# Optimization experiments

Hardware: AMD Instinct MI355X
Metric: run time of the kernel (lower is better)

## Reference

```python
import jax, jax.numpy as jnp
import numpy as np

B, H, S = 64, 1024, 512
MIN_VAL, MAX_VAL = -1.0, 1.0
EPS = 1e-8  # torch F.cosine_similarity default eps


def setup_inputs() -> dict:
    key = jax.random.key(0)
    k1, k2, k3 = jax.random.split(key, 3)
    tree_state = jax.random.normal(k1, (B, H), dtype=jnp.float32)
    seq_states = jax.random.normal(k2, (B, H, S), dtype=jnp.float32)
    # binary validity mask (float, as it is multiplied in)
    seq_mask = (jax.random.uniform(k3, (B, S)) < 0.9).astype(jnp.float32)
    return {"tree_state": tree_state, "seq_states": seq_states, "seq_mask": seq_mask}


def reference(tree_state, seq_states, seq_mask):
    # scan over the seq axis; carry h: (B, H)
    xs = (jnp.transpose(seq_states, (2, 0, 1)), seq_mask.T)  # (S,B,H), (S,B)

    def step(h, x):
        s, m = x  # s: (B,H), m: (B,)
        dot = jnp.sum(h * s, axis=-1)  # (B,)
        denom = jnp.maximum(
            jnp.linalg.norm(h, axis=-1) * jnp.linalg.norm(s, axis=-1), EPS
        )
        cos = (dot / denom)[:, None]  # (B,1)
        h_new = jnp.clip(h + (s - h * cos) * m[:, None], MIN_VAL, MAX_VAL)
        return h_new, None

    h, _ = jax.lax.scan(step, tree_state, xs)
    return h
```

## Files before the change

kernel.cpp:

```cpp
#include <hip/hip_runtime.h>


#define NB 64
#define NH 1024
#define NS 512
#define EL 16

typedef float v4f __attribute__((ext_vector_type(4)));

template <int CTRL>
__device__ __forceinline__ float dpp_add(float x) {
  int s = __builtin_amdgcn_update_dpp(0, __builtin_bit_cast(int, x), CTRL, 0xf,
                                      0xf, true);
  return x + __builtin_bit_cast(float, s);
}

__device__ __forceinline__ float readlane_f(float v, int lane) {
  return __builtin_bit_cast(
      float, __builtin_amdgcn_readlane(__builtin_bit_cast(int, v), lane));
}

__device__ __forceinline__ void wave_sum2(float& a, float& b) {
  a = dpp_add<0x111>(a); b = dpp_add<0x111>(b);
  a = dpp_add<0x112>(a); b = dpp_add<0x112>(b);
  a = dpp_add<0x114>(a); b = dpp_add<0x114>(b);
  a = dpp_add<0x118>(a); b = dpp_add<0x118>(b);
  a = dpp_add<0x142>(a); b = dpp_add<0x142>(b);
  a = dpp_add<0x143>(a); b = dpp_add<0x143>(b);
  a = readlane_f(a, 63);
  b = readlane_f(b, 63);
}

__device__ __forceinline__ void wave_sum4(float& a, float& b, float& c,
                                          float& d) {
  a = dpp_add<0x111>(a); b = dpp_add<0x111>(b); c = dpp_add<0x111>(c); d = dpp_add<0x111>(d);
  a = dpp_add<0x112>(a); b = dpp_add<0x112>(b); c = dpp_add<0x112>(c); d = dpp_add<0x112>(d);
  a = dpp_add<0x114>(a); b = dpp_add<0x114>(b); c = dpp_add<0x114>(c); d = dpp_add<0x114>(d);
  a = dpp_add<0x118>(a); b = dpp_add<0x118>(b); c = dpp_add<0x118>(c); d = dpp_add<0x118>(d);
  a = dpp_add<0x142>(a); b = dpp_add<0x142>(b); c = dpp_add<0x142>(c); d = dpp_add<0x142>(d);
  a = dpp_add<0x143>(a); b = dpp_add<0x143>(b); c = dpp_add<0x143>(c); d = dpp_add<0x143>(d);
  a = readlane_f(a, 63);
  b = readlane_f(b, 63);
  c = readlane_f(c, 63);
  d = readlane_f(d, 63);
}

#define GLD4(dst, p, OFFSTR)                                   \
  asm volatile("global_load_dwordx4 %0, %1, off" OFFSTR        \
               : "=v"(dst)                                     \
               : "v"(p))
#define GLD1(dst, p)                                           \
  asm volatile("global_load_dword %0, %1, off" : "=v"(dst) : "v"(p))

#define ISSUE16(buf)                       \
  do {                                     \
    GLD4(buf[0], p0, " offset:-4096");     \
    GLD4(buf[1], p0, " offset:-2048");     \
    GLD4(buf[2], p0, "");                  \
    GLD4(buf[3], p0, " offset:2048");      \
    GLD4(buf[4], p1, " offset:-4096");     \
    GLD4(buf[5], p1, " offset:-2048");     \
    GLD4(buf[6], p1, "");                  \
    GLD4(buf[7], p1, " offset:2048");      \
    GLD4(buf[8], p2, " offset:-4096");     \
    GLD4(buf[9], p2, " offset:-2048");     \
    GLD4(buf[10], p2, "");                 \
    GLD4(buf[11], p2, " offset:2048");     \
    GLD4(buf[12], p3, " offset:-4096");    \
    GLD4(buf[13], p3, " offset:-2048");    \
    GLD4(buf[14], p3, "");                 \
    GLD4(buf[15], p3, " offset:2048");     \
    p0 += 4; p1 += 4; p2 += 4; p3 += 4;    \
  } while (0)

#define WAITPIN(buf, N)                                             \
  do {                                                              \
    asm volatile("s_waitcnt vmcnt(" N ")"                           \
                 : "+v"(buf[0]), "+v"(buf[1]), "+v"(buf[2]),        \
                   "+v"(buf[3]), "+v"(buf[4]), "+v"(buf[5]),        \
                   "+v"(buf[6]), "+v"(buf[7]));                     \
    asm volatile("s_waitcnt vmcnt(" N ")"                           \
                 : "+v"(buf[8]), "+v"(buf[9]), "+v"(buf[10]),       \
                   "+v"(buf[11]), "+v"(buf[12]), "+v"(buf[13]),     \
                   "+v"(buf[14]), "+v"(buf[15]));                   \
  } while (0)

__global__ __launch_bounds__(64, 1) void otsu_scan_kernel(
    const float* __restrict__ tree,
    const float* __restrict__ seq,
    const float* __restrict__ mask,
    float* __restrict__ out) {
  const int b = blockIdx.x;
  const int lane = threadIdx.x;

  const float* hrow = tree + b * NH + lane * EL;
  v4f hv[4];
  GLD4(hv[0], hrow, "");
  GLD4(hv[1], hrow, " offset:16");
  GLD4(hv[2], hrow, " offset:32");
  GLD4(hv[3], hrow, " offset:48");
  float m8[8];
  {
    const float* mp = mask + b * NS + lane;
    GLD1(m8[0], mp);
    GLD1(m8[1], mp + 64);
    GLD1(m8[2], mp + 128);
    GLD1(m8[3], mp + 192);
    GLD1(m8[4], mp + 256);
    GLD1(m8[5], mp + 320);
    GLD1(m8[6], mp + 384);
    GLD1(m8[7], mp + 448);
  }
  asm volatile("s_waitcnt vmcnt(0)"
               : "+v"(hv[0]), "+v"(hv[1]), "+v"(hv[2]), "+v"(hv[3]),
                 "+v"(m8[0]), "+v"(m8[1]), "+v"(m8[2]), "+v"(m8[3]),
                 "+v"(m8[4]), "+v"(m8[5]), "+v"(m8[6]), "+v"(m8[7]));

  float h[EL];
#pragma unroll
  for (int k = 0; k < 4; ++k) {
    h[4 * k + 0] = hv[k].x;
    h[4 * k + 1] = hv[k].y;
    h[4 * k + 2] = hv[k].z;
    h[4 * k + 3] = hv[k].w;
  }

  const float* srow = seq + (size_t)b * NH * NS + (size_t)(lane * EL) * NS;
  const float* p0 = srow + 2 * NS;
  const float* p1 = srow + 6 * NS;
  const float* p2 = srow + 10 * NS;
  const float* p3 = srow + 14 * NS;

  v4f bufA[16], bufB[16];

  auto process4 = [&](const v4f* buf, float mv, int lbase, bool has_t0) {
    float fA0 = 0.f, fA1 = 0.f, fA2 = 0.f, fA3 = 0.f;
    float fB0 = 0.f, fB1 = 0.f, fB2 = 0.f, fB3 = 0.f;
#pragma unroll
    for (int i = 0; i < EL; i += 2) {
      fA0 = fmaf(buf[i][0], buf[i][0], fA0);
      fA1 = fmaf(buf[i][1], buf[i][1], fA1);
      fA2 = fmaf(buf[i][2], buf[i][2], fA2);
      fA3 = fmaf(buf[i][3], buf[i][3], fA3);
      fB0 = fmaf(buf[i + 1][0], buf[i + 1][0], fB0);
      fB1 = fmaf(buf[i + 1][1], buf[i + 1][1], fB1);
      fB2 = fmaf(buf[i + 1][2], buf[i + 1][2], fB2);
      fB3 = fmaf(buf[i + 1][3], buf[i + 1][3], fB3);
    }
    float s2g[4];
    s2g[0] = fA0 + fB0;
    s2g[1] = fA1 + fB1;
    s2g[2] = fA2 + fB2;
    s2g[3] = fA3 + fB3;
    wave_sum4(s2g[0], s2g[1], s2g[2], s2g[3]);

#pragma unroll
    for (int j = 0; j < 4; ++j) {
      const float m = readlane_f(mv, lbase + j);
      if (m != 0.0f) {
        float d0 = 0.f, d1 = 0.f, d2 = 0.f, d3 = 0.f;
        float e0 = 0.f, e1 = 0.f, e2 = 0.f, e3 = 0.f;
#pragma unroll
        for (int i = 0; i < EL; i += 4) {
          const float sA = buf[i + 0][j];
          const float sB = buf[i + 1][j];
          const float sC = buf[i + 2][j];
          const float sD = buf[i + 3][j];
          d0 = fmaf(h[i + 0], sA, d0);
          e0 = fmaf(h[i + 0], h[i + 0], e0);
          d1 = fmaf(h[i + 1], sB, d1);
          e1 = fmaf(h[i + 1], h[i + 1], e1);
          d2 = fmaf(h[i + 2], sC, d2);
          e2 = fmaf(h[i + 2], h[i + 2], e2);
          d3 = fmaf(h[i + 3], sD, d3);
          e3 = fmaf(h[i + 3], h[i + 3], e3);
        }
        float dot = (d0 + d1) + (d2 + d3);
        float hh = (e0 + e1) + (e2 + e3);
        wave_sum2(dot, hh);
        const float p = fmaxf(hh * s2g[j], 1e-16f);
        const float c = dot * __builtin_amdgcn_rsqf(p);
        const float a = 1.0f - c;
#pragma unroll
        for (int i = 0; i < EL; ++i)
          h[i] = __builtin_amdgcn_fmed3f(fmaf(h[i], a, buf[i][j]), -1.0f,
                                         1.0f);
      } else if (has_t0 && j == 0) {
#pragma unroll
        for (int i = 0; i < EL; ++i)
          h[i] = __builtin_amdgcn_fmed3f(h[i], -1.0f, 1.0f);
      }
    }
  };

  ISSUE16(bufA);

#pragma unroll
  for (int sg = 0; sg < 8; ++sg) {
    const float mv = m8[sg];
    const int nIter = (sg == 7) ? 7 : 8;
    for (int it = 0; it < nIter; ++it) {
      const int lbase = 8 * it;
      ISSUE16(bufB);
      WAITPIN(bufA, "16");
      process4(bufA, mv, lbase, sg == 0 && it == 0);
      ISSUE16(bufA);
      WAITPIN(bufB, "16");
      process4(bufB, mv, lbase + 4, false);
    }
  }
  {
    const float mv = m8[7];
    ISSUE16(bufB);
    WAITPIN(bufA, "16");
    process4(bufA, mv, 56, false);
    WAITPIN(bufB, "0");
    process4(bufB, mv, 60, false);
  }

  float* orow = out + b * NH + lane * EL;
#pragma unroll
  for (int i = 0; i < EL / 4; ++i) {
    float4 v;
    v.x = h[4 * i + 0];
    v.y = h[4 * i + 1];
    v.z = h[4 * i + 2];
    v.w = h[4 * i + 3];
    *(float4*)(orow + 4 * i) = v;
  }
}

extern "C" void kernel_launch(void* const* d_in, const int* in_sizes, int n_in,
                              void* d_out, int out_size, void* d_ws,
                              size_t ws_size, hipStream_t stream) {
  const float* tree = (const float*)d_in[0];
  const float* seq = (const float*)d_in[1];
  const float* mask = (const float*)d_in[2];
  float* out = (float*)d_out;
  otsu_scan_kernel<<<dim3(NB), dim3(64), 0, stream>>>(tree, seq, mask, out);
}
```

Baseline: 312.1 us.

## Stage seq tiles through LDS transpose with buffer-load ring pipeline

Replaces direct per-lane strided global loads with buffer loads into an 8-deep register ring. Each tile is written transposed into a double-buffered LDS region, so every timestep's H-slice is read back as contiguous ds_read_b128 per lane. The compute step now folds the s-norm into the same pass as the dot products, using a 3-way wave reduction per step. The mask is packed into bits so a step's compute can be skipped. This is meant to improve global memory coalescing and overlap load latency with the serial scan, at the cost of LDS traffic and more complex wait-count scheduling.

```diff
diff --git a/kernel.cpp b/kernel.cpp
--- a/kernel.cpp
+++ b/kernel.cpp
@@ -4,9 +4,11 @@
 #define NB 64
 #define NH 1024
 #define NS 512
-#define EL 16
 
 typedef float v4f __attribute__((ext_vector_type(4)));
+typedef int v4i __attribute__((ext_vector_type(4)));
+
+template <int N> struct ic { static constexpr int value = N; };
 
 template <int CTRL>
 __device__ __forceinline__ float dpp_add(float x) {
@@ -20,29 +22,16 @@
       float, __builtin_amdgcn_readlane(__builtin_bit_cast(int, v), lane));
 }
 
-__device__ __forceinline__ void wave_sum2(float& a, float& b) {
-  a = dpp_add<0x111>(a); b = dpp_add<0x111>(b);
-  a = dpp_add<0x112>(a); b = dpp_add<0x112>(b);
-  a = dpp_add<0x114>(a); b = dpp_add<0x114>(b);
-  a = dpp_add<0x118>(a); b = dpp_add<0x118>(b);
-  a = dpp_add<0x142>(a); b = dpp_add<0x142>(b);
-  a = dpp_add<0x143>(a); b = dpp_add<0x143>(b);
-  a = readlane_f(a, 63);
-  b = readlane_f(b, 63);
-}
-
-__device__ __forceinline__ void wave_sum4(float& a, float& b, float& c,
-                                          float& d) {
-  a = dpp_add<0x111>(a); b = dpp_add<0x111>(b); c = dpp_add<0x111>(c); d = dpp_add<0x111>(d);
-  a = dpp_add<0x112>(a); b = dpp_add<0x112>(b); c = dpp_add<0x112>(c); d = dpp_add<0x112>(d);
-  a = dpp_add<0x114>(a); b = dpp_add<0x114>(b); c = dpp_add<0x114>(c); d = dpp_add<0x114>(d);
-  a = dpp_add<0x118>(a); b = dpp_add<0x118>(b); c = dpp_add<0x118>(c); d = dpp_add<0x118>(d);
-  a = dpp_add<0x142>(a); b = dpp_add<0x142>(b); c = dpp_add<0x142>(c); d = dpp_add<0x142>(d);
-  a = dpp_add<0x143>(a); b = dpp_add<0x143>(b); c = dpp_add<0x143>(c); d = dpp_add<0x143>(d);
+__device__ __forceinline__ void wave_sum3(float& a, float& b, float& c) {
+  a = dpp_add<0x111>(a); b = dpp_add<0x111>(b); c = dpp_add<0x111>(c);
+  a = dpp_add<0x112>(a); b = dpp_add<0x112>(b); c = dpp_add<0x112>(c);
+  a = dpp_add<0x114>(a); b = dpp_add<0x114>(b); c = dpp_add<0x114>(c);
+  a = dpp_add<0x118>(a); b = dpp_add<0x118>(b); c = dpp_add<0x118>(c);
+  a = dpp_add<0x142>(a); b = dpp_add<0x142>(b); c = dpp_add<0x142>(c);
+  a = dpp_add<0x143>(a); b = dpp_add<0x143>(b); c = dpp_add<0x143>(c);
   a = readlane_f(a, 63);
   b = readlane_f(b, 63);
   c = readlane_f(c, 63);
-  d = readlane_f(d, 63);
 }
 
 #define GLD4(dst, p, OFFSTR)                                   \
@@ -52,56 +41,116 @@
 #define GLD1(dst, p)                                           \
   asm volatile("global_load_dword %0, %1, off" : "=v"(dst) : "v"(p))
 
-#define ISSUE16(buf)                       \
-  do {                                     \
-    GLD4(buf[0], p0, " offset:-4096");     \
-    GLD4(buf[1], p0, " offset:-2048");     \
-    GLD4(buf[2], p0, "");                  \
-    GLD4(buf[3], p0, " offset:2048");      \
-    GLD4(buf[4], p1, " offset:-4096");     \
-    GLD4(buf[5], p1, " offset:-2048");     \
-    GLD4(buf[6], p1, "");                  \
-    GLD4(buf[7], p1, " offset:2048");      \
-    GLD4(buf[8], p2, " offset:-4096");     \
-    GLD4(buf[9], p2, " offset:-2048");     \
-    GLD4(buf[10], p2, "");                 \
-    GLD4(buf[11], p2, " offset:2048");     \
-    GLD4(buf[12], p3, " offset:-4096");    \
-    GLD4(buf[13], p3, " offset:-2048");    \
-    GLD4(buf[14], p3, "");                 \
-    GLD4(buf[15], p3, " offset:2048");     \
-    p0 += 4; p1 += 4; p2 += 4; p3 += 4;    \
-  } while (0)
-
-#define WAITPIN(buf, N)                                             \
-  do {                                                              \
-    asm volatile("s_waitcnt vmcnt(" N ")"                           \
-                 : "+v"(buf[0]), "+v"(buf[1]), "+v"(buf[2]),        \
-                   "+v"(buf[3]), "+v"(buf[4]), "+v"(buf[5]),        \
-                   "+v"(buf[6]), "+v"(buf[7]));                     \
-    asm volatile("s_waitcnt vmcnt(" N ")"                           \
-                 : "+v"(buf[8]), "+v"(buf[9]), "+v"(buf[10]),       \
-                   "+v"(buf[11]), "+v"(buf[12]), "+v"(buf[13]),     \
-                   "+v"(buf[14]), "+v"(buf[15]));                   \
-  } while (0)
+template <int IMM>
+__device__ __forceinline__ void dsr128(v4f& d, unsigned a) {
+  asm volatile("ds_read_b128 %[d], %[a] offset:%[o]"
+               : [d] "=v"(d)
+               : [a] "v"(a), [o] "n"(IMM));
+}
+template <int IMM>
+__device__ __forceinline__ void dsw32(unsigned a, float v) {
+  asm volatile("ds_write_b32 %[a], %[v] offset:%[o]" ::[a] "v"(a), [v] "v"(v),
+               [o] "n"(IMM));
+}
+__device__ __forceinline__ void bld4(v4f& d, unsigned voff, v4i srsrc,
+                                     unsigned so) {
+  asm volatile("buffer_load_dwordx4 %[d], %[vo], %[rs], %[so] offen"
+               : [d] "=v"(d)
+               : [vo] "v"(voff), [rs] "s"(srsrc), [so] "s"(so));
+}
+
+#define VMW12(rg)                                                          \
+  asm volatile("s_waitcnt vmcnt(12)"                                       \
+               : "+v"((rg)[0]), "+v"((rg)[1]), "+v"((rg)[2]), "+v"((rg)[3]))
+#define LGK0(sv)                                                           \
+  asm volatile("s_waitcnt lgkmcnt(0)"                                      \
+               : "+v"((sv)[0]), "+v"((sv)[1]), "+v"((sv)[2]), "+v"((sv)[3]))
+
+template <int T>
+__device__ __forceinline__ void read_issue(unsigned rb, v4f (&sv)[4]) {
+  dsr128<T * 4096 + 0>(sv[0], rb);
+  dsr128<T * 4096 + 1024>(sv[1], rb);
+  dsr128<T * 4096 + 2048>(sv[2], rb);
+  dsr128<T * 4096 + 3072>(sv[3], rb);
+}
+
+template <int S>
+__device__ __forceinline__ void stage_write(unsigned wb, v4f (&rg)[4]) {
+#define DSWUJ(u, j) dsw32<(j) * 4096 + 256 * S + 64 * (u)>(wb, rg[u][j])
+  DSWUJ(0, 0); DSWUJ(0, 1); DSWUJ(0, 2); DSWUJ(0, 3);
+  DSWUJ(1, 0); DSWUJ(1, 1); DSWUJ(1, 2); DSWUJ(1, 3);
+  DSWUJ(2, 0); DSWUJ(2, 1); DSWUJ(2, 2); DSWUJ(2, 3);
+  DSWUJ(3, 0); DSWUJ(3, 1); DSWUJ(3, 2); DSWUJ(3, 3);
+#undef DSWUJ
+}
+
+__device__ __forceinline__ void stage_load(v4f (&rg)[4], unsigned voff,
+                                           v4i srsrc, unsigned& so) {
+  bld4(rg[0], voff, srsrc, so); so += 32768u;
+  bld4(rg[1], voff, srsrc, so); so += 32768u;
+  bld4(rg[2], voff, srsrc, so); so += 32768u;
+  bld4(rg[3], voff, srsrc, so); so += 32768u;
+}
+
+__device__ __forceinline__ void compute_step(float (&h)[16],
+                                             const v4f (&sv)[4]) {
+  float d0 = 0.f, d1 = 0.f, d2 = 0.f, d3 = 0.f;
+  float e0 = 0.f, e1 = 0.f, e2 = 0.f, e3 = 0.f;
+  float f0 = 0.f, f1 = 0.f, f2 = 0.f, f3 = 0.f;
+#pragma unroll
+  for (int m = 0; m < 4; ++m) {
+    const float s0 = sv[m][0], s1 = sv[m][1], s2 = sv[m][2], s3 = sv[m][3];
+    d0 = fmaf(h[4 * m + 0], s0, d0);
+    e0 = fmaf(h[4 * m + 0], h[4 * m + 0], e0);
+    f0 = fmaf(s0, s0, f0);
+    d1 = fmaf(h[4 * m + 1], s1, d1);
+    e1 = fmaf(h[4 * m + 1], h[4 * m + 1], e1);
+    f1 = fmaf(s1, s1, f1);
+    d2 = fmaf(h[4 * m + 2], s2, d2);
+    e2 = fmaf(h[4 * m + 2], h[4 * m + 2], e2);
+    f2 = fmaf(s2, s2, f2);
+    d3 = fmaf(h[4 * m + 3], s3, d3);
+    e3 = fmaf(h[4 * m + 3], h[4 * m + 3], e3);
+    f3 = fmaf(s3, s3, f3);
+  }
+  float dot = (d0 + d1) + (d2 + d3);
+  float hh = (e0 + e1) + (e2 + e3);
+  float ss = (f0 + f1) + (f2 + f3);
+  wave_sum3(dot, hh, ss);
+  const float p = fmaxf(hh * ss, 1e-16f);
+  const float c = dot * __builtin_amdgcn_rsqf(p);
+  const float a = 1.0f - c;
+#pragma unroll
+  for (int m = 0; m < 4; ++m) {
+    h[4 * m + 0] =
+        __builtin_amdgcn_fmed3f(fmaf(h[4 * m + 0], a, sv[m][0]), -1.0f, 1.0f);
+    h[4 * m + 1] =
+        __builtin_amdgcn_fmed3f(fmaf(h[4 * m + 1], a, sv[m][1]), -1.0f, 1.0f);
+    h[4 * m + 2] =
+        __builtin_amdgcn_fmed3f(fmaf(h[4 * m + 2], a, sv[m][2]), -1.0f, 1.0f);
+    h[4 * m + 3] =
+        __builtin_amdgcn_fmed3f(fmaf(h[4 * m + 3], a, sv[m][3]), -1.0f, 1.0f);
+  }
+}
 
 __global__ __launch_bounds__(64, 1) void otsu_scan_kernel(
     const float* __restrict__ tree,
     const float* __restrict__ seq,
     const float* __restrict__ mask,
     float* __restrict__ out) {
+  __shared__ float lds[2 * 16 * 1024];
   const int b = blockIdx.x;
-  const int lane = threadIdx.x;
-
-  const float* hrow = tree + b * NH + lane * EL;
+  const int l = threadIdx.x;
+
+  const float* hrow = tree + b * NH + 4 * l;
   v4f hv[4];
   GLD4(hv[0], hrow, "");
-  GLD4(hv[1], hrow, " offset:16");
-  GLD4(hv[2], hrow, " offset:32");
-  GLD4(hv[3], hrow, " offset:48");
+  GLD4(hv[1], hrow, " offset:1024");
+  GLD4(hv[2], hrow, " offset:2048");
+  GLD4(hv[3], hrow, " offset:3072");
   float m8[8];
   {
-    const float* mp = mask + b * NS + lane;
+    const float* mp = mask + b * NS + l;
     GLD1(m8[0], mp);
     GLD1(m8[1], mp + 64);
     GLD1(m8[2], mp + 128);
@@ -116,117 +165,102 @@
                  "+v"(m8[0]), "+v"(m8[1]), "+v"(m8[2]), "+v"(m8[3]),
                  "+v"(m8[4]), "+v"(m8[5]), "+v"(m8[6]), "+v"(m8[7]));
 
-  float h[EL];
-#pragma unroll
-  for (int k = 0; k < 4; ++k) {
-    h[4 * k + 0] = hv[k].x;
-    h[4 * k + 1] = hv[k].y;
-    h[4 * k + 2] = hv[k].z;
-    h[4 * k + 3] = hv[k].w;
-  }
-
-  const float* srow = seq + (size_t)b * NH * NS + (size_t)(lane * EL) * NS;
-  const float* p0 = srow + 2 * NS;
-  const float* p1 = srow + 6 * NS;
-  const float* p2 = srow + 10 * NS;
-  const float* p3 = srow + 14 * NS;
-
-  v4f bufA[16], bufB[16];
-
-  auto process4 = [&](const v4f* buf, float mv, int lbase, bool has_t0) {
-    float fA0 = 0.f, fA1 = 0.f, fA2 = 0.f, fA3 = 0.f;
-    float fB0 = 0.f, fB1 = 0.f, fB2 = 0.f, fB3 = 0.f;
-#pragma unroll
-    for (int i = 0; i < EL; i += 2) {
-      fA0 = fmaf(buf[i][0], buf[i][0], fA0);
-      fA1 = fmaf(buf[i][1], buf[i][1], fA1);
-      fA2 = fmaf(buf[i][2], buf[i][2], fA2);
-      fA3 = fmaf(buf[i][3], buf[i][3], fA3);
-      fB0 = fmaf(buf[i + 1][0], buf[i + 1][0], fB0);
-      fB1 = fmaf(buf[i + 1][1], buf[i + 1][1], fB1);
-      fB2 = fmaf(buf[i + 1][2], buf[i + 1][2], fB2);
-      fB3 = fmaf(buf[i + 1][3], buf[i + 1][3], fB3);
-    }
-    float s2g[4];
-    s2g[0] = fA0 + fB0;
-    s2g[1] = fA1 + fB1;
-    s2g[2] = fA2 + fB2;
-    s2g[3] = fA3 + fB3;
-    wave_sum4(s2g[0], s2g[1], s2g[2], s2g[3]);
-
-#pragma unroll
-    for (int j = 0; j < 4; ++j) {
-      const float m = readlane_f(mv, lbase + j);
-      if (m != 0.0f) {
-        float d0 = 0.f, d1 = 0.f, d2 = 0.f, d3 = 0.f;
-        float e0 = 0.f, e1 = 0.f, e2 = 0.f, e3 = 0.f;
-#pragma unroll
-        for (int i = 0; i < EL; i += 4) {
-          const float sA = buf[i + 0][j];
-          const float sB = buf[i + 1][j];
-          const float sC = buf[i + 2][j];
-          const float sD = buf[i + 3][j];
-          d0 = fmaf(h[i + 0], sA, d0);
-          e0 = fmaf(h[i + 0], h[i + 0], e0);
-          d1 = fmaf(h[i + 1], sB, d1);
-          e1 = fmaf(h[i + 1], h[i + 1], e1);
-          d2 = fmaf(h[i + 2], sC, d2);
-          e2 = fmaf(h[i + 2], h[i + 2], e2);
-          d3 = fmaf(h[i + 3], sD, d3);
-          e3 = fmaf(h[i + 3], h[i + 3], e3);
-        }
-        float dot = (d0 + d1) + (d2 + d3);
-        float hh = (e0 + e1) + (e2 + e3);
-        wave_sum2(dot, hh);
-        const float p = fmaxf(hh * s2g[j], 1e-16f);
-        const float c = dot * __builtin_amdgcn_rsqf(p);
-        const float a = 1.0f - c;
-#pragma unroll
-        for (int i = 0; i < EL; ++i)
-          h[i] = __builtin_amdgcn_fmed3f(fmaf(h[i], a, buf[i][j]), -1.0f,
-                                         1.0f);
-      } else if (has_t0 && j == 0) {
-#pragma unroll
-        for (int i = 0; i < EL; ++i)
-          h[i] = __builtin_amdgcn_fmed3f(h[i], -1.0f, 1.0f);
-      }
-    }
-  };
-
-  ISSUE16(bufA);
-
-#pragma unroll
-  for (int sg = 0; sg < 8; ++sg) {
-    const float mv = m8[sg];
-    const int nIter = (sg == 7) ? 7 : 8;
-    for (int it = 0; it < nIter; ++it) {
-      const int lbase = 8 * it;
-      ISSUE16(bufB);
-      WAITPIN(bufA, "16");
-      process4(bufA, mv, lbase, sg == 0 && it == 0);
-      ISSUE16(bufA);
-      WAITPIN(bufB, "16");
-      process4(bufB, mv, lbase + 4, false);
-    }
-  }
+  float h[16];
+#pragma unroll
+  for (int m = 0; m < 4; ++m) {
+    h[4 * m + 0] = hv[m][0];
+    h[4 * m + 1] = hv[m][1];
+    h[4 * m + 2] = hv[m][2];
+    h[4 * m + 3] = hv[m][3];
+  }
+
+  unsigned mbits = 0u;
+#pragma unroll
+  for (int i = 0; i < 8; ++i)
+    if (m8[i] != 0.0f) mbits |= (1u << i);
+
+  if (!(__builtin_amdgcn_readlane((int)mbits, 0) & 1)) {
+#pragma unroll
+    for (int i = 0; i < 16; ++i)
+      h[i] = __builtin_amdgcn_fmed3f(h[i], -1.0f, 1.0f);
+  }
+
+  v4i srsrc;
   {
-    const float mv = m8[7];
-    ISSUE16(bufB);
-    WAITPIN(bufA, "16");
-    process4(bufA, mv, 56, false);
-    WAITPIN(bufB, "0");
-    process4(bufB, mv, 60, false);
-  }
-
-  float* orow = out + b * NH + lane * EL;
-#pragma unroll
-  for (int i = 0; i < EL / 4; ++i) {
+    const unsigned long long base =
+        (unsigned long long)(seq + (size_t)b * NH * NS);
+    srsrc[0] = (int)(unsigned)(base & 0xffffffffull);
+    srsrc[1] = (int)(unsigned)(base >> 32);
+    srsrc[2] = NH * NS * 4;
+    srsrc[3] = 0x00020000;
+  }
+  const unsigned voff = (unsigned)((l >> 2) * 2048 + (l & 3) * 16);
+  const unsigned lb = (unsigned)(unsigned long long)(&lds[0]);
+  const unsigned rb0 = lb + 16u * (unsigned)l;
+  const unsigned wb0 = lb + (unsigned)((l & 3) * 16384 + (l >> 2) * 4);
+  unsigned so = 0u;
+
+  v4f ring[8][4];
+  v4f sval[2][4];
+
+  stage_load(ring[0], voff, srsrc, so);
+  stage_load(ring[1], voff, srsrc, so);
+  stage_load(ring[2], voff, srsrc, so);
+  stage_load(ring[3], voff, srsrc, so);
+#define PSTEP(v)                                              \
+  do {                                                        \
+    VMW12(ring[(v) & 7]);                                     \
+    stage_write<(v)>(wb0, ring[(v) & 7]);                     \
+    stage_load(ring[((v) + 4) & 7], voff, srsrc, so);         \
+    if ((v) == 11) so -= 2097088u;     \
+  } while (0)
+  PSTEP(0);  PSTEP(1);  PSTEP(2);  PSTEP(3);
+  PSTEP(4);  PSTEP(5);  PSTEP(6);  PSTEP(7);
+  PSTEP(8);  PSTEP(9);  PSTEP(10); PSTEP(11);
+  PSTEP(12); PSTEP(13); PSTEP(14); PSTEP(15);
+#undef PSTEP
+
+  read_issue<0>(rb0, sval[0]);
+
+  unsigned rb_cur = rb0;
+  unsigned wb_cur = wb0 ^ 0x10000u;
+
+#pragma unroll 1
+  for (int g = 0; g < 32; ++g) {
+    const int lbase = (16 * g) & 63;
+    const int msh = g >> 2;
+    auto step = [&](auto sc) {
+      constexpr int S = decltype(sc)::value;
+      LGK0(sval[S & 1]);
+      if constexpr (S < 15) read_issue<S + 1>(rb_cur, sval[(S + 1) & 1]);
+      const unsigned mw =
+          (unsigned)__builtin_amdgcn_readlane((int)mbits, lbase + S);
+      if ((mw >> msh) & 1u) compute_step(h, sval[S & 1]);
+      VMW12(ring[S & 7]);
+      stage_write<S>(wb_cur, ring[S & 7]);
+      stage_load(ring[(S + 4) & 7], voff, srsrc, so);
+      if constexpr (S == 11) { so -= 2097088u; }
+      if constexpr (S == 15) { read_issue<0>(rb_cur ^ 0x10000u, sval[0]); }
+    };
+    step(ic<0>{});  step(ic<1>{});  step(ic<2>{});  step(ic<3>{});
+    step(ic<4>{});  step(ic<5>{});  step(ic<6>{});  step(ic<7>{});
+    step(ic<8>{});  step(ic<9>{});  step(ic<10>{}); step(ic<11>{});
+    step(ic<12>{}); step(ic<13>{}); step(ic<14>{}); step(ic<15>{});
+    rb_cur ^= 0x10000u;
+    wb_cur ^= 0x10000u;
+  }
+
+  asm volatile("s_waitcnt vmcnt(0) lgkmcnt(0)" ::: "memory");
+
+  float* orow = out + b * NH + 4 * l;
+#pragma unroll
+  for (int m = 0; m < 4; ++m) {
     float4 v;
-    v.x = h[4 * i + 0];
-    v.y = h[4 * i + 1];
-    v.z = h[4 * i + 2];
-    v.w = h[4 * i + 3];
-    *(float4*)(orow + 4 * i) = v;
+    v.x = h[4 * m + 0];
+    v.y = h[4 * m + 1];
+    v.z = h[4 * m + 2];
+    v.w = h[4 * m + 3];
+    *(float4*)(orow + 256 * m) = v;
   }
 }
 
```

New measurement: 316.4 us. About the same (+1.4%).
